# Kernel optimization log

Hardware: AMD Instinct MI355X
Metric: run time of the kernel (lower is better)

Reference implementation:

```python
import jax, jax.numpy as jnp
import numpy as np

B, T, D, H, DH, COUT, PRED, K, DFF = 16, 512, 512, 8, 64, 7, 96, 16, 2048
LOW_FREQ = 1
LN_EPS = 1e-5


def _next_fast_len(n):
    while True:
        m = n
        for p in (2, 3, 5):
            while m % p == 0:
                m //= p
        if m == 1:
            return n
        n += 1


def conv1d_fft(f, g, axis=1):
    # FFT cross-correlation, matching torch conv1d_fft (roll + tail slice)
    N = f.shape[axis]
    M = g.shape[axis]
    L = _next_fast_len(N + M - 1)
    Ff = jnp.fft.rfft(f, n=L, axis=axis)
    Fg = jnp.fft.rfft(g, n=L, axis=axis)
    out = jnp.fft.irfft(Ff * jnp.conj(Fg), n=L, axis=axis)
    out = jnp.roll(out, -1, axis=axis)
    return jax.lax.slice_in_dim(out, L - N, L, axis=axis)


def es_weights(sw, T_):
    alpha = jax.nn.sigmoid(sw)                       # (h,1)
    powers = jnp.arange(T_, dtype=jnp.float32)       # (T,)
    init_w = alpha ** (powers + 1.0)                 # (h,T)
    w = (1.0 - alpha) * alpha ** powers[::-1]        # (h,T)
    return init_w.T[None, :, :, None], w.T[None, :, :, None]  # (1,T,h,1)


def exponential_smoothing(values, v0, sw, aux_values=None):
    b, t, h, d = values.shape
    init_w, w = es_weights(sw, t)
    out = init_w * v0 + conv1d_fft(values, w, axis=1)
    if aux_values is not None:
        alpha = jax.nn.sigmoid(sw).reshape(1, 1, h, 1)
        aux_w = w / jnp.maximum(1.0 - alpha, 1e-6) * alpha
        out = out + conv1d_fft(aux_values, aux_w, axis=1)
    return out


def fourier_extrapolate(x, pred_len, k, low_freq=LOW_FREQ):
    b, t, d = x.shape
    x_freq = jnp.fft.rfft(x, axis=1)                 # (b, t//2+1, d)
    hi_end = x_freq.shape[1] - 1 if t % 2 == 0 else x_freq.shape[1]
    x_freq_high = x_freq[:, low_freq:hi_end]
    k_ = k if (k is not None and k < t // 2) else max(1, hi_end - low_freq)
    k_ = min(k_, x_freq_high.shape[1])
    mag = jnp.abs(x_freq_high).transpose(0, 2, 1)    # (b,d,F)
    _, idx = jax.lax.top_k(mag, k_)                  # (b,d,k)
    idx = idx.transpose(0, 2, 1) + low_freq          # (b,k,d)
    x_topk = jnp.take_along_axis(x_freq, idx, axis=1)
    freqs = jnp.fft.rfftfreq(t).astype(jnp.float32)
    f_topk = jnp.take_along_axis(
        jnp.broadcast_to(freqs[None, :, None], (b, freqs.shape[0], d)), idx, axis=1)
    x_ex = jnp.concatenate([x_topk, jnp.conj(x_topk)], axis=1)   # (b,2k,d)
    f_ex = jnp.concatenate([f_topk, -f_topk], axis=1)
    tt = jnp.arange(t + pred_len, dtype=jnp.float32)[None, None, :, None]
    amp = (jnp.abs(x_ex) / t)[:, :, None, :]
    phase = jnp.angle(x_ex)[:, :, None, :]
    x_time = amp * jnp.cos(2.0 * jnp.pi * f_ex[:, :, None, :] * tt + phase)
    return x_time.sum(axis=1)                        # (b, t+pred_len, d)


def layer_norm(x, g, b, eps=LN_EPS):
    mu = x.mean(-1, keepdims=True)
    var = ((x - mu) ** 2).mean(-1, keepdims=True)
    return (x - mu) / jnp.sqrt(var + eps) * g + b


def _forward(res, level, Wi, bi, z0, v0_g, sw_g, Wo, bo, W1, W2,
             g1, b1_ln, g2, b2_ln, Wg, bg, Ws, bs, v0_l, sw_l):
    b, t, _ = res.shape
    # season block
    season = fourier_extrapolate(res, PRED, K)               # (b, t+PRED, d)
    res1 = res - season[:, :t]
    # growth block
    v = (res1 @ Wi.T + bi).reshape(b, t, H, DH)
    v = jnp.concatenate([jnp.broadcast_to(z0[None, None], (b, 1, H, DH)), v], axis=1)
    diffs = v[:, 1:] - v[:, :-1]                             # (b,t,H,DH)
    sm = exponential_smoothing(diffs, v0_g, sw_g)
    gr = jnp.concatenate([jnp.broadcast_to(v0_g, (b, 1, H, DH)), sm], axis=1)
    growth = gr.reshape(b, t + 1, H * DH) @ Wo.T + bo        # (b,t+1,d)
    # residual path
    h = layer_norm(res1 - growth[:, 1:], g1, b1_ln)
    ff = jax.nn.relu(h @ W1.T) @ W2.T
    h = layer_norm(h + ff, g2, b2_ln)
    # level block
    gp = growth[:, 1:t + 1] @ Wg.T + bg                      # (b,t,COUT)
    sp = season[:, :t] @ Ws.T + bs
    es_in = (level - sp)[..., None]                          # (b,t,COUT,1)
    lvl = exponential_smoothing(es_in, v0_l, sw_l, aux_values=gp[..., None])[..., 0]
    return h, lvl, growth, season


def setup_inputs() -> dict:
    key = jax.random.key(0)
    ks = jax.random.split(key, 20)
    s = 0.02
    return {
        "res": jax.random.normal(ks[0], (B, T, D), jnp.float32),
        "level": jax.random.normal(ks[1], (B, T, COUT), jnp.float32),
        "Wi": jax.random.normal(ks[2], (H * DH, D), jnp.float32) * s,
        "bi": jnp.zeros((H * DH,), jnp.float32),
        "z0": jax.random.normal(ks[3], (H, DH), jnp.float32),
        "v0_g": jax.random.normal(ks[4], (1, 1, H, DH), jnp.float32),
        "sw_g": jax.random.normal(ks[5], (H, 1), jnp.float32),
        "Wo": jax.random.normal(ks[6], (D, H * DH), jnp.float32) * s,
        "bo": jnp.zeros((D,), jnp.float32),
        "W1": jax.random.normal(ks[7], (DFF, D), jnp.float32) * s,
        "W2": jax.random.normal(ks[8], (D, DFF), jnp.float32) * s,
        "g1": jnp.ones((D,), jnp.float32),
        "b1_ln": jnp.zeros((D,), jnp.float32),
        "g2": jnp.ones((D,), jnp.float32),
        "b2_ln": jnp.zeros((D,), jnp.float32),
        "Wg": jax.random.normal(ks[9], (COUT, D), jnp.float32) * s,
        "bg": jnp.zeros((COUT,), jnp.float32),
        "Ws": jax.random.normal(ks[10], (COUT, D), jnp.float32) * s,
        "bs": jnp.zeros((COUT,), jnp.float32),
        "v0_l": jax.random.normal(ks[11], (1, 1, COUT, 1), jnp.float32),
        "sw_l": jax.random.normal(ks[12], (COUT, 1), jnp.float32),
    }


def reference(res, level, Wi, bi, z0, v0_g, sw_g, Wo, bo, W1, W2,
              g1, b1_ln, g2, b2_ln, Wg, bg, Ws, bs, v0_l, sw_l):
    return _forward(res, level, Wi, bi, z0, v0_g, sw_g, Wo, bo, W1, W2,
                    g1, b1_ln, g2, b2_ln, Wg, bg, Ws, bs, v0_l, sw_l)
```

## Files before the change

kernel.cpp:

```cpp
#include <hip/hip_runtime.h>
#include <math.h>

#define Bn 16
#define Tn 512
#define Dn 512
#define COUTn 7
#define PREDn 96

using f32x4 = __attribute__((ext_vector_type(4))) float;
using bf16x8 = __attribute__((ext_vector_type(8))) __bf16;

__device__ __forceinline__ unsigned short f2b(float f) {
  unsigned int u = __float_as_uint(f);
  u += 0x7fff + ((u >> 16) & 1);
  return (unsigned short)(u >> 16);
}

__device__ __forceinline__ void gld16(const void* g, void* l) {
  __builtin_amdgcn_global_load_lds(
      (const __attribute__((address_space(1))) void*)g,
      (__attribute__((address_space(3))) void*)l, 16, 0, 0);
}

__global__ __launch_bounds__(256) void cvt_bf16(
    const float* __restrict__ in, unsigned short* __restrict__ out, int n) {
  int i = (blockIdx.x * 256 + threadIdx.x) * 4;
  if (i + 3 < n) {
    float4 v = *reinterpret_cast<const float4*>(&in[i]);
    ushort4 o;
    o.x = f2b(v.x); o.y = f2b(v.y); o.z = f2b(v.z); o.w = f2b(v.w);
    *reinterpret_cast<ushort4*>(&out[i]) = o;
  }
}

__global__ __launch_bounds__(256) void twiddle_init2(
    unsigned short* __restrict__ twc_b, unsigned short* __restrict__ tws_b,
    double* __restrict__ tabw, float* __restrict__ c512,
    float* __restrict__ s512) {
  int idx = blockIdx.x * 256 + threadIdx.x;
  int k = idx >> 9, t = idx & 511;
  int m = (k * t) & 511;
  double ang = (double)m * (M_PI / 256.0);
  twc_b[idx] = f2b((float)cos(ang));
  tws_b[idx] = f2b((float)sin(ang));
  if (idx < 512) {
    double a2 = (double)idx * (M_PI / 256.0);
    c512[idx] = (float)cos(a2);
    s512[idx] = (float)sin(a2);
    tabw[2 * idx] = cos(a2);
    tabw[2 * idx + 1] = -sin(a2);
  }
}

__global__ __launch_bounds__(256) void transpose_cvt(
    const float* __restrict__ res, unsigned short* __restrict__ resT) {
  __shared__ unsigned short tile[64][65];
  int b = blockIdx.z;
  int t0 = blockIdx.y * 64, d0 = blockIdx.x * 64;
  int tid = threadIdx.x;
  int c = tid & 63, r4 = (tid >> 6) * 16;
#pragma unroll
  for (int i = 0; i < 16; ++i) {
    int t = t0 + r4 + i;
    tile[r4 + i][c] = f2b(res[((size_t)(b * 512 + t)) * 512 + d0 + c]);
  }
  __syncthreads();
#pragma unroll
  for (int i = 0; i < 16; ++i) {
    int d = d0 + r4 + i;
    resT[((size_t)(b * 512 + d)) * 512 + t0 + c] = tile[c][r4 + i];
  }
}

__global__ __launch_bounds__(256) void screen_mfma(
    const unsigned short* __restrict__ twc_b,
    const unsigned short* __restrict__ tws_b,
    const unsigned short* __restrict__ resT, float* __restrict__ mag) {
  __shared__ unsigned short lAc[2048];
  __shared__ unsigned short lAs[2048];
  __shared__ unsigned short lB[4096];
  int tid = threadIdx.x;
  int wv = tid >> 6, lane = tid & 63;
  int b = blockIdx.z;
  int k0 = blockIdx.y * 64;
  int d0 = blockIdx.x * 128;

  int rA = wv * 16 + (lane >> 2);
  int rB0 = wv * 32 + (lane >> 2);
  int rB1 = rB0 + 16;
  int kk = (lane & 3) * 8;
  int kkA = kk ^ (((rA >> 1) & 3) << 3);
  int kkB0 = kk ^ (((rB0 >> 1) & 3) << 3);
  int kkB1 = kk ^ (((rB1 >> 1) & 3) << 3);
  const unsigned short* ac = twc_b + (size_t)(k0 + rA) * 512 + kkA;
  const unsigned short* as = tws_b + (size_t)(k0 + rA) * 512 + kkA;
  const unsigned short* bb0 = resT + ((size_t)(b * 512 + d0 + rB0)) * 512 + kkB0;
  const unsigned short* bb1 = resT + ((size_t)(b * 512 + d0 + rB1)) * 512 + kkB1;
  unsigned short* dAc = &lAc[wv * 512];
  unsigned short* dAs = &lAs[wv * 512];
  unsigned short* dB0 = &lB[wv * 1024];
  unsigned short* dB1 = &lB[wv * 1024 + 512];

  int frow = lane & 15, fk = (lane >> 4) * 8;
  int ia[4], ib[2];
#pragma unroll
  for (int i = 0; i < 4; ++i) {
    int r = i * 16 + frow;
    ia[i] = r * 32 + (fk ^ (((r >> 1) & 3) << 3));
  }
#pragma unroll
  for (int j = 0; j < 2; ++j) {
    int r = wv * 32 + j * 16 + frow;
    ib[j] = r * 32 + (fk ^ (((r >> 1) & 3) << 3));
  }

  f32x4 accR[4][2] = {};
  f32x4 accI[4][2] = {};
  for (int t0 = 0; t0 < 512; t0 += 32) {
    gld16(ac + t0, dAc);
    gld16(as + t0, dAs);
    gld16(bb0 + t0, dB0);
    gld16(bb1 + t0, dB1);
    __syncthreads();
    bf16x8 afc[4], afs[4], bw[2];
#pragma unroll
    for (int i = 0; i < 4; ++i) {
      afc[i] = *reinterpret_cast<const bf16x8*>(&lAc[ia[i]]);
      afs[i] = *reinterpret_cast<const bf16x8*>(&lAs[ia[i]]);
    }
#pragma unroll
    for (int j = 0; j < 2; ++j)
      bw[j] = *reinterpret_cast<const bf16x8*>(&lB[ib[j]]);
#pragma unroll
    for (int i = 0; i < 4; ++i)
#pragma unroll
      for (int j = 0; j < 2; ++j) {
        accR[i][j] = __builtin_amdgcn_mfma_f32_16x16x32_bf16(
            afc[i], bw[j], accR[i][j], 0, 0, 0);
        accI[i][j] = __builtin_amdgcn_mfma_f32_16x16x32_bf16(
            afs[i], bw[j], accI[i][j], 0, 0, 0);
      }
    __syncthreads();
  }

  int ccol = lane & 15, crow4 = (lane >> 4) * 4;
#pragma unroll
  for (int i = 0; i < 4; ++i) {
    int kb = k0 + i * 16 + crow4;
#pragma unroll
    for (int j = 0; j < 2; ++j) {
      int d = d0 + wv * 32 + j * 16 + ccol;
#pragma unroll
      for (int r = 0; r < 4; ++r) {
        float re = accR[i][j][r], im = accI[i][j][r];
        mag[((size_t)(b * 256 + kb + r)) * 512 + d] = re * re + im * im;
      }
    }
  }
}

__global__ __launch_bounds__(64) void cand32(
    const float* __restrict__ mag, int* __restrict__ cand) {
  int blk = blockIdx.x;
  int b = blk >> 9;
  int d = blk & 511;
  int lane = threadIdx.x;
  float m2[4];
#pragma unroll
  for (int i = 0; i < 4; ++i) {
    int k = 1 + lane + 64 * i;
    m2[i] = (k <= 255) ? mag[((size_t)(b * 256 + k)) * 512 + d] : -1.f;
  }
  for (int j = 0; j < 32; ++j) {
    float bm = -2.f; int bk = 1 << 20;
#pragma unroll
    for (int i = 0; i < 4; ++i) {
      int k = 1 + lane + 64 * i;
      if (m2[i] > bm || (m2[i] == bm && k < bk)) { bm = m2[i]; bk = k; }
    }
    for (int o = 32; o > 0; o >>= 1) {
      float om = __shfl_down(bm, o, 64);
      int ok = __shfl_down(bk, o, 64);
      if (om > bm || (om == bm && ok < bk)) { bm = om; bk = ok; }
    }
    bk = __shfl(bk, 0, 64);
    if (lane == 0) cand[((size_t)(b * 32 + j)) * 512 + d] = bk;
#pragma unroll
    for (int i = 0; i < 4; ++i) {
      int k = 1 + lane + 64 * i;
      if (k == bk) m2[i] = -1.f;
    }
  }
}

__global__ __launch_bounds__(512) void refine32(
    const float* __restrict__ res, const int* __restrict__ cand,
    const double* __restrict__ tabw, int* __restrict__ kidx,
    float* __restrict__ cjb, float* __restrict__ sjb) {
  int b = blockIdx.y;
  int d0 = blockIdx.x * 16;
  int tid = threadIdx.x;
  __shared__ float colbuf[512][17];
  for (int idx = tid; idx < 8192; idx += 512) {
    int t = idx >> 4, c = idx & 15;
    colbuf[t][c] = res[((size_t)(b * 512 + t)) * 512 + d0 + c];
  }
  __syncthreads();

  int j = tid & 31, c = tid >> 5;
  int k = cand[((size_t)(b * 32 + j)) * 512 + d0 + c];
  double wr = tabw[2 * k], wi = tabw[2 * k + 1];
  double zr = 1.0, zi = 0.0, ar = 0.0, ai = 0.0;
#pragma unroll 4
  for (int t = 0; t < 512; ++t) {
    double x = (double)colbuf[t][c];
    ar = fma(x, zr, ar);
    ai = fma(x, zi, ai);
    double nzr = fma(zr, wr, -zi * wi);
    double nzi = fma(zr, wi, zi * wr);
    zr = nzr; zi = nzi;
  }
  double m2 = ar * ar + ai * ai;
  float cjv = (float)(ar * (2.0 / 512.0));
  float sjv = (float)(ai * (2.0 / 512.0));
  for (int jo = 0; jo < 16; ++jo) {
    double bm = m2; int bk = k;
#pragma unroll
    for (int o = 16; o > 0; o >>= 1) {
      double om = __shfl_xor(bm, o, 32);
      int ok = __shfl_xor(bk, o, 32);
      if (om > bm || (om == bm && ok < bk)) { bm = om; bk = ok; }
    }
    if (k == bk) {
      size_t o = ((size_t)(b * 16 + jo)) * 512 + d0 + c;
      kidx[o] = k; cjb[o] = cjv; sjb[o] = sjv;
      m2 = -1.0;
    }
  }
}

__global__ __launch_bounds__(512) void synth_kernel(
    const int* __restrict__ kidx, const float* __restrict__ cjb,
    const float* __restrict__ sjb, const float* __restrict__ c512,
    const float* __restrict__ s512, const float* __restrict__ res,
    float* __restrict__ season, unsigned short* __restrict__ res1b) {
  int b = blockIdx.y;
  int t0 = blockIdx.x * 16;
  int d = threadIdx.x;

  __shared__ float ct[512], st[512];
  ct[d] = c512[d];
  st[d] = s512[d];
  __syncthreads();

  int kk[16];
  float cw[16], sw[16];
#pragma unroll
  for (int j = 0; j < 16; ++j) {
    size_t o = ((size_t)(b * 16 + j)) * 512 + d;
    kk[j] = kidx[o];
    cw[j] = cjb[o];
    sw[j] = sjb[o];
  }

  for (int tt = 0; tt < 16; ++tt) {
    int t = t0 + tt;
    if (t >= Tn + PREDn) break;
    float acc = 0.f;
#pragma unroll
    for (int j = 0; j < 16; ++j) {
      int m = (kk[j] * t) & 511;
      acc += cw[j] * ct[m] - sw[j] * st[m];
    }
    season[((size_t)(b * (Tn + PREDn) + t)) * 512 + d] = acc;
    if (t < Tn) {
      size_t o = ((size_t)(b * Tn + t)) * 512 + d;
      res1b[o] = f2b(res[o] - acc);
    }
  }
}

template <int MODE>
__global__ __launch_bounds__(256) void gemm_mfma(
    const unsigned short* __restrict__ A, const unsigned short* __restrict__ W,
    const float* __restrict__ bias, float* __restrict__ C,
    unsigned short* __restrict__ Cb, int M, int N, int Kd) {
  __shared__ unsigned short lA[4096];
  __shared__ unsigned short lB[4096];
  int tid = threadIdx.x;
  int wv = tid >> 6, lane = tid & 63;
  int m0 = blockIdx.y * 128, n0 = blockIdx.x * 128;
  int wr = (wv >> 1) * 64, wc = (wv & 1) * 64;

  int rA0 = wv * 32 + (lane >> 2);
  int rA1 = rA0 + 16;
  int kk = (lane & 3) * 8;
  int kk0 = kk ^ (((rA0 >> 1) & 3) << 3);
  int kk1 = kk ^ (((rA1 >> 1) & 3) << 3);
  int gmA0 = m0 + rA0; if (gmA0 > M - 1) gmA0 = M - 1;
  int gmA1 = m0 + rA1; if (gmA1 > M - 1) gmA1 = M - 1;
  const unsigned short* a0 = A + (size_t)gmA0 * Kd + kk0;
  const unsigned short* a1 = A + (size_t)gmA1 * Kd + kk1;
  const unsigned short* b0 = W + (size_t)(n0 + rA0) * Kd + kk0;
  const unsigned short* b1 = W + (size_t)(n0 + rA1) * Kd + kk1;
  unsigned short* dA0 = &lA[wv * 1024];
  unsigned short* dA1 = &lA[wv * 1024 + 512];
  unsigned short* dB0 = &lB[wv * 1024];
  unsigned short* dB1 = &lB[wv * 1024 + 512];

  int frow = lane & 15, fk = (lane >> 4) * 8;
  int ia[4], ib[4];
#pragma unroll
  for (int i = 0; i < 4; ++i) {
    int r = wr + i * 16 + frow;
    ia[i] = r * 32 + (fk ^ (((r >> 1) & 3) << 3));
    int rb = wc + i * 16 + frow;
    ib[i] = rb * 32 + (fk ^ (((rb >> 1) & 3) << 3));
  }

  f32x4 acc[4][4] = {};

  for (int k0 = 0; k0 < Kd; k0 += 32) {
    gld16(a0 + k0, dA0);
    gld16(a1 + k0, dA1);
    gld16(b0 + k0, dB0);
    gld16(b1 + k0, dB1);
    __syncthreads();
    bf16x8 af[4], bw[4];
#pragma unroll
    for (int i = 0; i < 4; ++i) {
      af[i] = *reinterpret_cast<const bf16x8*>(&lA[ia[i]]);
      bw[i] = *reinterpret_cast<const bf16x8*>(&lB[ib[i]]);
    }
#pragma unroll
    for (int i = 0; i < 4; ++i)
#pragma unroll
      for (int j = 0; j < 4; ++j)
        acc[i][j] = __builtin_amdgcn_mfma_f32_16x16x32_bf16(
            af[i], bw[j], acc[i][j], 0, 0, 0);
    __syncthreads();
  }

  int ccol = lane & 15, crow4 = (lane >> 4) * 4;
#pragma unroll
  for (int i = 0; i < 4; ++i) {
    int gm0 = m0 + wr + i * 16 + crow4;
#pragma unroll
    for (int j = 0; j < 4; ++j) {
      int gn = n0 + wc + j * 16 + ccol;
      float bv = 0.f;
      if (MODE == 0) bv = bias[gn];
#pragma unroll
      for (int r = 0; r < 4; ++r) {
        int gm = gm0 + r;
        if (gm < M) {
          size_t o = (size_t)gm * N + gn;
          float v = acc[i][j][r] + bv;
          if (MODE == 1) Cb[o] = f2b(fmaxf(v, 0.f));
          else if (MODE == 2) C[o] += v;
          else C[o] = v;
        }
      }
    }
  }
}

__global__ __launch_bounds__(256) void ema_gA(
    const float* __restrict__ v, const float* __restrict__ z0,
    const float* __restrict__ sw_g, float* __restrict__ tmp,
    float* __restrict__ sumend) {
  int g = blockIdx.x * 256 + threadIdx.x;
  int hd = g & 511;
  int ch = (g >> 9) & 7;
  int b = g >> 12;
  int h = hd >> 6;
  float alpha = 1.f / (1.f + expf(-sw_g[h]));
  float om = 1.f - alpha;
  int t0 = ch * 64;
  float prev = (t0 == 0) ? z0[hd] : v[((size_t)(b * 512 + t0 - 1)) * 512 + hd];
  float s = 0.f;
  for (int i = 0; i < 64; ++i) {
    float cur = v[((size_t)(b * 512 + t0 + i)) * 512 + hd];
    s = alpha * s + om * (cur - prev);
    prev = cur;
    tmp[((size_t)(b * 512 + t0 + i)) * 512 + hd] = s;
  }
  sumend[((size_t)(b * 512 + hd)) * 8 + ch] = s;
}

__global__ __launch_bounds__(256) void ema_gB(
    const float* __restrict__ sumend, const float* __restrict__ v0_g,
    const float* __restrict__ sw_g, float* __restrict__ carry,
    unsigned short* __restrict__ grb) {
  int g = blockIdx.x * 256 + threadIdx.x;
  int hd = g & 511, b = g >> 9, h = hd >> 6;
  float alpha = 1.f / (1.f + expf(-sw_g[h]));
  float A64 = exp2f(64.f * log2f(alpha));
  float cin = v0_g[hd];
  grb[((size_t)(b * 513)) * 512 + hd] = f2b(cin);
  for (int ch = 0; ch < 8; ++ch) {
    carry[((size_t)(b * 512 + hd)) * 8 + ch] = cin;
    cin = A64 * cin + sumend[((size_t)(b * 512 + hd)) * 8 + ch];
  }
}

__global__ __launch_bounds__(256) void ema_gC(
    const float* __restrict__ tmp, const float* __restrict__ carry,
    const float* __restrict__ sw_g, unsigned short* __restrict__ grb) {
  int g = blockIdx.x * 256 + threadIdx.x;
  int hd = g & 511;
  int t = (g >> 9) & 511;
  int b = g >> 18;
  int h = hd >> 6;
  float alpha = 1.f / (1.f + expf(-sw_g[h]));
  int ch = t >> 6, i = t & 63;
  float Ai = exp2f((float)(i + 1) * log2f(alpha));
  float s = tmp[g] + Ai * carry[((size_t)(b * 512 + hd)) * 8 + ch];
  grb[((size_t)(b * 513 + t + 1)) * 512 + hd] = f2b(s);
}

__global__ __launch_bounds__(256) void ln0_kernel(
    const float* __restrict__ res, const float* __restrict__ season,
    const float* __restrict__ growth, const float* __restrict__ g,
    const float* __restrict__ bvec, float* __restrict__ h1,
    unsigned short* __restrict__ h1b) {
  int row = blockIdx.x, b = row >> 9, t = row & 511;
  int tid = threadIdx.x;
  const float* xr = res + (size_t)row * 512;
  const float* sr = season + ((size_t)(b * (Tn + PREDn) + t)) * 512;
  const float* gr = growth + ((size_t)(b * (Tn + 1) + t + 1)) * 512;
  float2 xv = *reinterpret_cast<const float2*>(&xr[tid * 2]);
  float2 sv = *reinterpret_cast<const float2*>(&sr[tid * 2]);
  float2 gv2 = *reinterpret_cast<const float2*>(&gr[tid * 2]);
  float v0 = xv.x - sv.x - gv2.x;
  float v1 = xv.y - sv.y - gv2.y;
  float s1 = v0 + v1;
  float s2 = v0 * v0 + v1 * v1;
  for (int o = 32; o > 0; o >>= 1) {
    s1 += __shfl_down(s1, o, 64);
    s2 += __shfl_down(s2, o, 64);
  }
  __shared__ float r1[4], r2[4];
  __shared__ float mu_s, rstd_s;
  int wv = tid >> 6, ln = tid & 63;
  if (ln == 0) { r1[wv] = s1; r2[wv] = s2; }
  __syncthreads();
  if (tid == 0) {
    float S1 = r1[0] + r1[1] + r1[2] + r1[3];
    float S2 = r2[0] + r2[1] + r2[2] + r2[3];
    float mu = S1 * (1.0f / 512.0f);
    float var = S2 * (1.0f / 512.0f) - mu * mu;
    mu_s = mu;
    rstd_s = rsqrtf(var + 1e-5f);
  }
  __syncthreads();
  float mu = mu_s, rstd = rstd_s;
  float2 gv = *reinterpret_cast<const float2*>(&g[tid * 2]);
  float2 bv = *reinterpret_cast<const float2*>(&bvec[tid * 2]);
  float o0 = (v0 - mu) * rstd * gv.x + bv.x;
  float o1 = (v1 - mu) * rstd * gv.y + bv.y;
  size_t o = (size_t)row * 512 + tid * 2;
  *reinterpret_cast<float2*>(&h1[o]) = make_float2(o0, o1);
  ushort2 hb; hb.x = f2b(o0); hb.y = f2b(o1);
  *reinterpret_cast<ushort2*>(&h1b[o]) = hb;
}

__global__ __launch_bounds__(256) void ln1_kernel(
    const float* __restrict__ X, const float* __restrict__ g,
    const float* __restrict__ bvec, float* __restrict__ out) {
  int row = blockIdx.x;
  int tid = threadIdx.x;
  const float* xr = X + (size_t)row * 512;
  float2 xv = *reinterpret_cast<const float2*>(&xr[tid * 2]);
  float v0 = xv.x, v1 = xv.y;
  float s1 = v0 + v1;
  float s2 = v0 * v0 + v1 * v1;
  for (int o = 32; o > 0; o >>= 1) {
    s1 += __shfl_down(s1, o, 64);
    s2 += __shfl_down(s2, o, 64);
  }
  __shared__ float r1[4], r2[4];
  __shared__ float mu_s, rstd_s;
  int wv = tid >> 6, ln = tid & 63;
  if (ln == 0) { r1[wv] = s1; r2[wv] = s2; }
  __syncthreads();
  if (tid == 0) {
    float S1 = r1[0] + r1[1] + r1[2] + r1[3];
    float S2 = r2[0] + r2[1] + r2[2] + r2[3];
    float mu = S1 * (1.0f / 512.0f);
    float var = S2 * (1.0f / 512.0f) - mu * mu;
    mu_s = mu;
    rstd_s = rsqrtf(var + 1e-5f);
  }
  __syncthreads();
  float mu = mu_s, rstd = rstd_s;
  float2 gv = *reinterpret_cast<const float2*>(&g[tid * 2]);
  float2 bv = *reinterpret_cast<const float2*>(&bvec[tid * 2]);
  float o0 = (v0 - mu) * rstd * gv.x + bv.x;
  float o1 = (v1 - mu) * rstd * gv.y + bv.y;
  *reinterpret_cast<float2*>(&out[(size_t)row * 512 + tid * 2]) =
      make_float2(o0, o1);
}

__global__ __launch_bounds__(64) void proj7_kernel(
    const float* __restrict__ X, int strB, int off,
    const float* __restrict__ Wc, const float* __restrict__ bc,
    float* __restrict__ outp) {
  int bt = blockIdx.x;
  int b = bt >> 9;
  int t = bt & 511;
  int lane = threadIdx.x;
  const float* row = X + ((size_t)(b * strB + off + t)) * 512;
  float x[8];
#pragma unroll
  for (int i = 0; i < 8; ++i) x[i] = row[lane + 64 * i];
#pragma unroll
  for (int c = 0; c < 7; ++c) {
    float s = 0.f;
#pragma unroll
    for (int i = 0; i < 8; ++i) s += x[i] * Wc[c * 512 + lane + 64 * i];
    for (int o = 32; o > 0; o >>= 1) s += __shfl_down(s, o, 64);
    if (lane == 0) outp[((size_t)bt) * 7 + c] = s + bc[c];
  }
}

__global__ __launch_bounds__(256) void lvl_scan(
    const float* __restrict__ level, const float* __restrict__ sp,
    const float* __restrict__ gp, const float* __restrict__ v0_l,
    const float* __restrict__ sw_l, float* __restrict__ out_lvl) {
  int blk = blockIdx.x;
  int b = blk / 7, c = blk % 7;
  int tid = threadIdx.x;
  float alpha = 1.f / (1.f + expf(-sw_l[c]));
  float om = 1.f - alpha;
  size_t i0 = ((size_t)(b * 512 + 2 * tid)) * 7 + c;
  size_t i1 = i0 + 7;
  float u0 = om * (level[i0] - sp[i0]) + alpha * gp[i0];
  float u1 = om * (level[i1] - sp[i1]) + alpha * gp[i1];
  __shared__ float As[256], Us[256];
  As[tid] = alpha * alpha;
  Us[tid] = alpha * u0 + u1;
  __syncthreads();
  for (int off = 1; off < 256; off <<= 1) {
    float Ap = 1.f, Up = 0.f;
    if (tid >= off) { Ap = As[tid - off]; Up = Us[tid - off]; }
    __syncthreads();
    if (tid >= off) {
      float Ac = As[tid], Uc = Us[tid];
      As[tid] = Ac * Ap;
      Us[tid] = Ac * Up + Uc;
    }
    __syncthreads();
  }
  float v0 = v0_l[c];
  float Aex = (tid == 0) ? 1.f : As[tid - 1];
  float Uex = (tid == 0) ? 0.f : Us[tid - 1];
  float sprev = Aex * v0 + Uex;
  float o0 = alpha * sprev + u0;
  float o1 = alpha * o0 + u1;
  out_lvl[i0] = o0;
  out_lvl[i1] = o1;
}

extern "C" void kernel_launch(void* const* d_in, const int* in_sizes, int n_in,
                              void* d_out, int out_size, void* d_ws,
                              size_t ws_size, hipStream_t stream) {
  const float* res = (const float*)d_in[0];
  const float* level = (const float*)d_in[1];
  const float* Wi = (const float*)d_in[2];
  const float* bi = (const float*)d_in[3];
  const float* z0 = (const float*)d_in[4];
  const float* v0_g = (const float*)d_in[5];
  const float* sw_g = (const float*)d_in[6];
  const float* Wo = (const float*)d_in[7];
  const float* bo = (const float*)d_in[8];
  const float* W1 = (const float*)d_in[9];
  const float* W2 = (const float*)d_in[10];
  const float* g1 = (const float*)d_in[11];
  const float* b1 = (const float*)d_in[12];
  const float* g2 = (const float*)d_in[13];
  const float* b2 = (const float*)d_in[14];
  const float* Wg = (const float*)d_in[15];
  const float* bg = (const float*)d_in[16];
  const float* Wse = (const float*)d_in[17];
  const float* bs = (const float*)d_in[18];
  const float* v0_l = (const float*)d_in[19];
  const float* sw_l = (const float*)d_in[20];

  float* out = (float*)d_out;
  float* out_h = out;
  float* out_lvl = out + 4194304;
  float* out_growth = out + 4251648;
  float* out_season = out + 8454144;

  float* wsf = (float*)d_ws;
  unsigned short* res1_b = (unsigned short*)wsf;
  unsigned short* h1_b = (unsigned short*)wsf;
  float* gpb = wsf;
  float* spb = wsf + 57344;
  unsigned short* resT_b = (unsigned short*)(wsf + 2097152);
  float* magb = wsf + 4194304;
  int* candb = (int*)(wsf + 6291456);
  unsigned short* twc_b = (unsigned short*)(wsf + 6553600);
  unsigned short* tws_b = (unsigned short*)(wsf + 6619136);
  float* vbuf = wsf + 2097152;
  unsigned short* grbuf_b = (unsigned short*)(wsf + 6291456);
  float* sumend = wsf + 8392704;
  float* carryb = wsf + 8458240;
  unsigned short* ff1_b = (unsigned short*)(wsf + 2097152);
  double* tabw = (double*)(wsf + 10485760);
  float* c512 = wsf + 10487808;
  float* s512 = wsf + 10488320;
  int* kidx = (int*)(wsf + 10488832);
  float* cjb = wsf + 10619904;
  float* sjb = wsf + 10750976;
  float* tmpb = wsf + 10485760;
  float* h1 = wsf + 10485760;
  unsigned short* Wi_b = (unsigned short*)(wsf + 14680064);
  unsigned short* Wo_b = (unsigned short*)(wsf + 14811136);
  unsigned short* W1_b = (unsigned short*)(wsf + 14942208);
  unsigned short* W2_b = (unsigned short*)(wsf + 15466496);

  hipLaunchKernelGGL(cvt_bf16, dim3(256), dim3(256), 0, stream, Wi, Wi_b, 262144);
  hipLaunchKernelGGL(cvt_bf16, dim3(256), dim3(256), 0, stream, Wo, Wo_b, 262144);
  hipLaunchKernelGGL(cvt_bf16, dim3(1024), dim3(256), 0, stream, W1, W1_b, 1048576);
  hipLaunchKernelGGL(cvt_bf16, dim3(1024), dim3(256), 0, stream, W2, W2_b, 1048576);

  hipLaunchKernelGGL(twiddle_init2, dim3(512), dim3(256), 0, stream,
                     twc_b, tws_b, tabw, c512, s512);
  hipLaunchKernelGGL(transpose_cvt, dim3(8, 8, 16), dim3(256), 0, stream,
                     res, resT_b);
  hipLaunchKernelGGL(screen_mfma, dim3(4, 4, 16), dim3(256), 0, stream,
                     twc_b, tws_b, resT_b, magb);
  hipLaunchKernelGGL(cand32, dim3(8192), dim3(64), 0, stream, magb, candb);
  hipLaunchKernelGGL(refine32, dim3(32, 16), dim3(512), 0, stream,
                     res, candb, tabw, kidx, cjb, sjb);
  hipLaunchKernelGGL(synth_kernel, dim3(38, 16), dim3(512), 0, stream,
                     kidx, cjb, sjb, c512, s512, res, out_season, res1_b);
  hipLaunchKernelGGL((gemm_mfma<0>), dim3(4, 64), dim3(256), 0, stream,
                     res1_b, Wi_b, bi, vbuf, (unsigned short*)nullptr,
                     8192, 512, 512);
  hipLaunchKernelGGL(ema_gA, dim3(256), dim3(256), 0, stream,
                     vbuf, z0, sw_g, tmpb, sumend);
  hipLaunchKernelGGL(ema_gB, dim3(32), dim3(256), 0, stream,
                     sumend, v0_g, sw_g, carryb, grbuf_b);
  hipLaunchKernelGGL(ema_gC, dim3(16384), dim3(256), 0, stream,
                     tmpb, carryb, sw_g, grbuf_b);
  hipLaunchKernelGGL((gemm_mfma<0>), dim3(4, 65), dim3(256), 0, stream,
                     grbuf_b, Wo_b, bo, out_growth, (unsigned short*)nullptr,
                     8208, 512, 512);
  hipLaunchKernelGGL(ln0_kernel, dim3(Bn * Tn), dim3(256), 0, stream,
                     res, out_season, out_growth, g1, b1, h1, h1_b);
  hipLaunchKernelGGL((gemm_mfma<1>), dim3(16, 64), dim3(256), 0, stream,
                     h1_b, W1_b, (const float*)nullptr, (float*)nullptr, ff1_b,
                     8192, 2048, 512);
  hipLaunchKernelGGL((gemm_mfma<2>), dim3(4, 64), dim3(256), 0, stream,
                     ff1_b, W2_b, (const float*)nullptr, h1,
                     (unsigned short*)nullptr, 8192, 512, 2048);
  hipLaunchKernelGGL(ln1_kernel, dim3(Bn * Tn), dim3(256), 0, stream,
                     h1, g2, b2, out_h);
  hipLaunchKernelGGL(proj7_kernel, dim3(Bn * Tn), dim3(64), 0, stream,
                     out_growth, Tn + 1, 1, Wg, bg, gpb);
  hipLaunchKernelGGL(proj7_kernel, dim3(Bn * Tn), dim3(64), 0, stream,
                     out_season, Tn + PREDn, 0, Wse, bs, spb);
  hipLaunchKernelGGL(lvl_scan, dim3(112), dim3(256), 0, stream,
                     level, spb, gpb, v0_l, sw_l, out_lvl);

  (void)in_sizes; (void)n_in; (void)out_size; (void)ws_size;
}
```

Baseline: 506.4 us.

## Double-buffer LDS in MFMA kernels, split-K W2 GEMM, narrower tiles, fuse proj7 launches

```diff
diff --git a/kernel.cpp b/kernel.cpp
--- a/kernel.cpp
+++ b/kernel.cpp
@@ -76,9 +76,9 @@
     const unsigned short* __restrict__ twc_b,
     const unsigned short* __restrict__ tws_b,
     const unsigned short* __restrict__ resT, float* __restrict__ mag) {
-  __shared__ unsigned short lAc[2048];
-  __shared__ unsigned short lAs[2048];
-  __shared__ unsigned short lB[4096];
+  __shared__ unsigned short lAc[2][2048];
+  __shared__ unsigned short lAs[2][2048];
+  __shared__ unsigned short lB[2][4096];
   int tid = threadIdx.x;
   int wv = tid >> 6, lane = tid & 63;
   int b = blockIdx.z;
@@ -96,10 +96,6 @@
   const unsigned short* as = tws_b + (size_t)(k0 + rA) * 512 + kkA;
   const unsigned short* bb0 = resT + ((size_t)(b * 512 + d0 + rB0)) * 512 + kkB0;
   const unsigned short* bb1 = resT + ((size_t)(b * 512 + d0 + rB1)) * 512 + kkB1;
-  unsigned short* dAc = &lAc[wv * 512];
-  unsigned short* dAs = &lAs[wv * 512];
-  unsigned short* dB0 = &lB[wv * 1024];
-  unsigned short* dB1 = &lB[wv * 1024 + 512];
 
   int frow = lane & 15, fk = (lane >> 4) * 8;
   int ia[4], ib[2];
@@ -116,21 +112,31 @@
 
   f32x4 accR[4][2] = {};
   f32x4 accI[4][2] = {};
-  for (int t0 = 0; t0 < 512; t0 += 32) {
-    gld16(ac + t0, dAc);
-    gld16(as + t0, dAs);
-    gld16(bb0 + t0, dB0);
-    gld16(bb1 + t0, dB1);
-    __syncthreads();
+
+  gld16(ac, &lAc[0][wv * 512]);
+  gld16(as, &lAs[0][wv * 512]);
+  gld16(bb0, &lB[0][wv * 1024]);
+  gld16(bb1, &lB[0][wv * 1024 + 512]);
+  __syncthreads();
+
+  int cur = 0;
+  for (int t = 0; t < 16; ++t) {
+    if (t + 1 < 16) {
+      int ko = (t + 1) * 32;
+      gld16(ac + ko, &lAc[cur ^ 1][wv * 512]);
+      gld16(as + ko, &lAs[cur ^ 1][wv * 512]);
+      gld16(bb0 + ko, &lB[cur ^ 1][wv * 1024]);
+      gld16(bb1 + ko, &lB[cur ^ 1][wv * 1024 + 512]);
+    }
     bf16x8 afc[4], afs[4], bw[2];
 #pragma unroll
     for (int i = 0; i < 4; ++i) {
-      afc[i] = *reinterpret_cast<const bf16x8*>(&lAc[ia[i]]);
-      afs[i] = *reinterpret_cast<const bf16x8*>(&lAs[ia[i]]);
+      afc[i] = *reinterpret_cast<const bf16x8*>(&lAc[cur][ia[i]]);
+      afs[i] = *reinterpret_cast<const bf16x8*>(&lAs[cur][ia[i]]);
     }
 #pragma unroll
     for (int j = 0; j < 2; ++j)
-      bw[j] = *reinterpret_cast<const bf16x8*>(&lB[ib[j]]);
+      bw[j] = *reinterpret_cast<const bf16x8*>(&lB[cur][ib[j]]);
 #pragma unroll
     for (int i = 0; i < 4; ++i)
 #pragma unroll
@@ -141,6 +147,7 @@
             afs[i], bw[j], accI[i][j], 0, 0, 0);
       }
     __syncthreads();
+    cur ^= 1;
   }
 
   int ccol = lane & 15, crow4 = (lane >> 4) * 4;
@@ -280,65 +287,94 @@
   }
 }
 
-template <int MODE>
+template <int MODE, int BN>
 __global__ __launch_bounds__(256) void gemm_mfma(
     const unsigned short* __restrict__ A, const unsigned short* __restrict__ W,
     const float* __restrict__ bias, float* __restrict__ C,
-    unsigned short* __restrict__ Cb, int M, int N, int Kd) {
-  __shared__ unsigned short lA[4096];
-  __shared__ unsigned short lB[4096];
+    unsigned short* __restrict__ Cb, int M, int N, int Kd, int ldk) {
+  constexpr int NF = BN / 32;
+  __shared__ unsigned short lA[2][4096];
+  __shared__ unsigned short lB[2][BN * 32];
   int tid = threadIdx.x;
   int wv = tid >> 6, lane = tid & 63;
-  int m0 = blockIdx.y * 128, n0 = blockIdx.x * 128;
-  int wr = (wv >> 1) * 64, wc = (wv & 1) * 64;
+  int m0 = blockIdx.y * 128, n0 = blockIdx.x * BN;
+  int koff = blockIdx.z * Kd;
+  int wr = (wv >> 1) * 64, wc = (wv & 1) * (BN / 2);
 
   int rA0 = wv * 32 + (lane >> 2);
   int rA1 = rA0 + 16;
   int kk = (lane & 3) * 8;
-  int kk0 = kk ^ (((rA0 >> 1) & 3) << 3);
-  int kk1 = kk ^ (((rA1 >> 1) & 3) << 3);
+  int kkA0 = kk ^ (((rA0 >> 1) & 3) << 3);
+  int kkA1 = kk ^ (((rA1 >> 1) & 3) << 3);
   int gmA0 = m0 + rA0; if (gmA0 > M - 1) gmA0 = M - 1;
   int gmA1 = m0 + rA1; if (gmA1 > M - 1) gmA1 = M - 1;
-  const unsigned short* a0 = A + (size_t)gmA0 * Kd + kk0;
-  const unsigned short* a1 = A + (size_t)gmA1 * Kd + kk1;
-  const unsigned short* b0 = W + (size_t)(n0 + rA0) * Kd + kk0;
-  const unsigned short* b1 = W + (size_t)(n0 + rA1) * Kd + kk1;
-  unsigned short* dA0 = &lA[wv * 1024];
-  unsigned short* dA1 = &lA[wv * 1024 + 512];
-  unsigned short* dB0 = &lB[wv * 1024];
-  unsigned short* dB1 = &lB[wv * 1024 + 512];
+  const unsigned short* a0 = A + (size_t)gmA0 * ldk + koff + kkA0;
+  const unsigned short* a1 = A + (size_t)gmA1 * ldk + koff + kkA1;
+
+  const unsigned short* b0;
+  const unsigned short* b1 = nullptr;
+  int dBo;
+  if constexpr (BN == 128) {
+    int rB0 = wv * 32 + (lane >> 2);
+    int rB1 = rB0 + 16;
+    int kkB0 = kk ^ (((rB0 >> 1) & 3) << 3);
+    int kkB1 = kk ^ (((rB1 >> 1) & 3) << 3);
+    b0 = W + (size_t)(n0 + rB0) * ldk + koff + kkB0;
+    b1 = W + (size_t)(n0 + rB1) * ldk + koff + kkB1;
+    dBo = wv * 1024;
+  } else {
+    int rB = wv * 16 + (lane >> 2);
+    int kkB = kk ^ (((rB >> 1) & 3) << 3);
+    b0 = W + (size_t)(n0 + rB) * ldk + koff + kkB;
+    dBo = wv * 512;
+  }
 
   int frow = lane & 15, fk = (lane >> 4) * 8;
-  int ia[4], ib[4];
+  int ia[4], ib[NF];
 #pragma unroll
   for (int i = 0; i < 4; ++i) {
     int r = wr + i * 16 + frow;
     ia[i] = r * 32 + (fk ^ (((r >> 1) & 3) << 3));
-    int rb = wc + i * 16 + frow;
-    ib[i] = rb * 32 + (fk ^ (((rb >> 1) & 3) << 3));
-  }
-
-  f32x4 acc[4][4] = {};
-
-  for (int k0 = 0; k0 < Kd; k0 += 32) {
-    gld16(a0 + k0, dA0);
-    gld16(a1 + k0, dA1);
-    gld16(b0 + k0, dB0);
-    gld16(b1 + k0, dB1);
-    __syncthreads();
-    bf16x8 af[4], bw[4];
-#pragma unroll
-    for (int i = 0; i < 4; ++i) {
-      af[i] = *reinterpret_cast<const bf16x8*>(&lA[ia[i]]);
-      bw[i] = *reinterpret_cast<const bf16x8*>(&lB[ib[i]]);
-    }
+  }
+#pragma unroll
+  for (int j = 0; j < NF; ++j) {
+    int r = wc + j * 16 + frow;
+    ib[j] = r * 32 + (fk ^ (((r >> 1) & 3) << 3));
+  }
+
+  f32x4 acc[4][NF] = {};
+  int nk = Kd >> 5;
+
+  gld16(a0, &lA[0][wv * 1024]);
+  gld16(a1, &lA[0][wv * 1024 + 512]);
+  gld16(b0, &lB[0][dBo]);
+  if constexpr (BN == 128) gld16(b1, &lB[0][dBo + 512]);
+  __syncthreads();
+
+  int cur = 0;
+  for (int t = 0; t < nk; ++t) {
+    if (t + 1 < nk) {
+      int ko = (t + 1) << 5;
+      gld16(a0 + ko, &lA[cur ^ 1][wv * 1024]);
+      gld16(a1 + ko, &lA[cur ^ 1][wv * 1024 + 512]);
+      gld16(b0 + ko, &lB[cur ^ 1][dBo]);
+      if constexpr (BN == 128) gld16(b1 + ko, &lB[cur ^ 1][dBo + 512]);
+    }
+    bf16x8 af[4], bw[NF];
 #pragma unroll
     for (int i = 0; i < 4; ++i)
-#pragma unroll
-      for (int j = 0; j < 4; ++j)
+      af[i] = *reinterpret_cast<const bf16x8*>(&lA[cur][ia[i]]);
+#pragma unroll
+    for (int j = 0; j < NF; ++j)
+      bw[j] = *reinterpret_cast<const bf16x8*>(&lB[cur][ib[j]]);
+#pragma unroll
+    for (int i = 0; i < 4; ++i)
+#pragma unroll
+      for (int j = 0; j < NF; ++j)
         acc[i][j] = __builtin_amdgcn_mfma_f32_16x16x32_bf16(
             af[i], bw[j], acc[i][j], 0, 0, 0);
     __syncthreads();
+    cur ^= 1;
   }
 
   int ccol = lane & 15, crow4 = (lane >> 4) * 4;
@@ -346,7 +382,7 @@
   for (int i = 0; i < 4; ++i) {
     int gm0 = m0 + wr + i * 16 + crow4;
 #pragma unroll
-    for (int j = 0; j < 4; ++j) {
+    for (int j = 0; j < NF; ++j) {
       int gn = n0 + wc + j * 16 + ccol;
       float bv = 0.f;
       if (MODE == 0) bv = bias[gn];
@@ -357,7 +393,7 @@
           size_t o = (size_t)gm * N + gn;
           float v = acc[i][j][r] + bv;
           if (MODE == 1) Cb[o] = f2b(fmaxf(v, 0.f));
-          else if (MODE == 2) C[o] += v;
+          else if (MODE == 3) atomicAdd(&C[o], v);
           else C[o] = v;
         }
       }
@@ -502,14 +538,22 @@
       make_float2(o0, o1);
 }
 
-__global__ __launch_bounds__(64) void proj7_kernel(
-    const float* __restrict__ X, int strB, int off,
-    const float* __restrict__ Wc, const float* __restrict__ bc,
-    float* __restrict__ outp) {
+__global__ __launch_bounds__(64) void proj7_dual(
+    const float* __restrict__ growth, const float* __restrict__ season,
+    const float* __restrict__ Wg, const float* __restrict__ bg,
+    const float* __restrict__ Wse, const float* __restrict__ bs,
+    float* __restrict__ gpb, float* __restrict__ spb) {
   int bt = blockIdx.x;
+  int which = blockIdx.y;
   int b = bt >> 9;
   int t = bt & 511;
   int lane = threadIdx.x;
+  const float* X = which ? season : growth;
+  int strB = which ? (Tn + PREDn) : (Tn + 1);
+  int off = which ? 0 : 1;
+  const float* Wc = which ? Wse : Wg;
+  const float* bc = which ? bs : bg;
+  float* outp = which ? spb : gpb;
   const float* row = X + ((size_t)(b * strB + off + t)) * 512;
   float x[8];
 #pragma unroll
@@ -637,32 +681,30 @@
                      res, candb, tabw, kidx, cjb, sjb);
   hipLaunchKernelGGL(synth_kernel, dim3(38, 16), dim3(512), 0, stream,
                      kidx, cjb, sjb, c512, s512, res, out_season, res1_b);
-  hipLaunchKernelGGL((gemm_mfma<0>), dim3(4, 64), dim3(256), 0, stream,
+  hipLaunchKernelGGL((gemm_mfma<0, 64>), dim3(8, 64, 1), dim3(256), 0, stream,
                      res1_b, Wi_b, bi, vbuf, (unsigned short*)nullptr,
-                     8192, 512, 512);
+                     8192, 512, 512, 512);
   hipLaunchKernelGGL(ema_gA, dim3(256), dim3(256), 0, stream,
                      vbuf, z0, sw_g, tmpb, sumend);
   hipLaunchKernelGGL(ema_gB, dim3(32), dim3(256), 0, stream,
                      sumend, v0_g, sw_g, carryb, grbuf_b);
   hipLaunchKernelGGL(ema_gC, dim3(16384), dim3(256), 0, stream,
                      tmpb, carryb, sw_g, grbuf_b);
-  hipLaunchKernelGGL((gemm_mfma<0>), dim3(4, 65), dim3(256), 0, stream,
+  hipLaunchKernelGGL((gemm_mfma<0, 64>), dim3(8, 65, 1), dim3(256), 0, stream,
                      grbuf_b, Wo_b, bo, out_growth, (unsigned short*)nullptr,
-                     8208, 512, 512);
+                     8208, 512, 512, 512);
   hipLaunchKernelGGL(ln0_kernel, dim3(Bn * Tn), dim3(256), 0, stream,
                      res, out_season, out_growth, g1, b1, h1, h1_b);
-  hipLaunchKernelGGL((gemm_mfma<1>), dim3(16, 64), dim3(256), 0, stream,
+  hipLaunchKernelGGL((gemm_mfma<1, 128>), dim3(16, 64, 1), dim3(256), 0, stream,
                      h1_b, W1_b, (const float*)nullptr, (float*)nullptr, ff1_b,
-                     8192, 2048, 512);
-  hipLaunchKernelGGL((gemm_mfma<2>), dim3(4, 64), dim3(256), 0, stream,
+                     8192, 2048, 512, 512);
+  hipLaunchKernelGGL((gemm_mfma<3, 64>), dim3(8, 64, 4), dim3(256), 0, stream,
                      ff1_b, W2_b, (const float*)nullptr, h1,
-                     (unsigned short*)nullptr, 8192, 512, 2048);
+                     (unsigned short*)nullptr, 8192, 512, 512, 2048);
   hipLaunchKernelGGL(ln1_kernel, dim3(Bn * Tn), dim3(256), 0, stream,
                      h1, g2, b2, out_h);
-  hipLaunchKernelGGL(proj7_kernel, dim3(Bn * Tn), dim3(64), 0, stream,
-                     out_growth, Tn + 1, 1, Wg, bg, gpb);
-  hipLaunchKernelGGL(proj7_kernel, dim3(Bn * Tn), dim3(64), 0, stream,
-                     out_season, Tn + PREDn, 0, Wse, bs, spb);
+  hipLaunchKernelGGL(proj7_dual, dim3(Bn * Tn, 2), dim3(64), 0, stream,
+                     out_growth, out_season, Wg, bg, Wse, bs, gpb, spb);
   hipLaunchKernelGGL(lvl_scan, dim3(112), dim3(256), 0, stream,
                      level, spb, gpb, v0_l, sw_l, out_lvl);
 
```

Measured after the change: 506.9 us. About the same (+0.1%).
